# Optimization experiments

Measured on AMD Instinct MI355X. Metric: run time of the kernel, lower is better.

Reference implementation:

```python
import jax, jax.numpy as jnp
import numpy as np

GRID = 112  # densepose predictor output resolution (hardcoded in forward)
D = 16      # CSE embedding dim (view(16, -1) in forward)


def setup_inputs() -> dict:
    key = jax.random.key(0)
    k1, k2 = jax.random.split(key)
    feats = jax.random.normal(k1, (2, D, GRID, GRID), dtype=jnp.float32)
    vertex_embeddings = jax.random.normal(k2, (27554, D), dtype=jnp.float32)
    return {"feats": feats, "vertex_embeddings": vertex_embeddings}


def reference(feats, vertex_embeddings):
    # feats: [B, 16, 112, 112]; vertex_embeddings: [M, 16]
    B = feats.shape[0]
    # per-pixel embeddings: [B, N, D] with N = 112*112 (matches feats[i].view(16,-1).T)
    x = feats.reshape(B, D, -1).transpose(0, 2, 1)
    x2 = jnp.sum(x * x, axis=-1, keepdims=True)            # [B, N, 1]
    v2 = jnp.sum(vertex_embeddings * vertex_embeddings, -1)  # [M]
    dist = x2 - 2.0 * jnp.einsum('bnd,md->bnm', x, vertex_embeddings) + v2
    dps = jnp.argmin(dist, axis=-1).reshape(B, GRID, GRID)  # [B, 112, 112] int
    return feats, dps
```

## Files before the change

kernel.cpp:

```cpp
#include <hip/hip_runtime.h>
#include <math.h>
#include <float.h>

#define GRIDP 112
#define NPIX (GRIDP * GRIDP)
#define D 16
#define TSA 3200
#define TSB 3072

typedef short s16x8 __attribute__((ext_vector_type(8)));
typedef float f32x16 __attribute__((ext_vector_type(16)));

__device__ inline unsigned short f2bf(float x) {
    unsigned u = __float_as_uint(x);
    u += 0x7fffu + ((u >> 16) & 1u);
    return (unsigned short)(u >> 16);
}
__device__ inline float bf2f(unsigned short b) { return __uint_as_float(((unsigned)b) << 16); }

#define MFMA __builtin_amdgcn_mfma_f32_32x32x16_bf16

__global__ __launch_bounds__(256) void prep_verts(
    const float* __restrict__ verts, char* __restrict__ abuf,
    float* __restrict__ v2p, int M, int Mtiles)
{
    int mp = blockIdx.x * 256 + threadIdx.x;
    if (mp >= Mtiles * 32) return;
    int tile = mp >> 5, row = mp & 31;
    float x[D]; float v2;
    if (mp < M) {
        const float4* r4 = (const float4*)(verts + (size_t)mp * D);
        float4 a = r4[0], b = r4[1], c = r4[2], d = r4[3];
        x[0]=a.x; x[1]=a.y; x[2]=a.z; x[3]=a.w;
        x[4]=b.x; x[5]=b.y; x[6]=b.z; x[7]=b.w;
        x[8]=c.x; x[9]=c.y; x[10]=c.z; x[11]=c.w;
        x[12]=d.x; x[13]=d.y; x[14]=d.z; x[15]=d.w;
        float s = 0.f;
#pragma unroll
        for (int e = 0; e < D; ++e) s = fmaf(x[e], x[e], s);
        v2 = s;
        v2p[mp] = s;
    } else {
#pragma unroll
        for (int e = 0; e < D; ++e) x[e] = 0.f;
        v2 = FLT_MAX;
    }
    size_t tb = (size_t)tile * TSA;
    int hv = (row >> 2) & 1, rv = (row & 3) + 4 * (row >> 3);
    *(float*)(abuf + tb + 3072 + hv * 64 + rv * 4) = v2;
#pragma unroll
    for (int e = 0; e < D; ++e) {
        float v = x[e];
        unsigned short t0 = f2bf(v);  float r1 = v - bf2f(t0);
        unsigned short t1 = f2bf(r1); float r2 = r1 - bf2f(t1);
        unsigned short t2 = f2bf(r2);
        size_t o = tb + (size_t)(e >> 3) * 512 + (size_t)row * 16 + (size_t)(e & 7) * 2;
        *(unsigned short*)(abuf + o)        = t0;
        *(unsigned short*)(abuf + o + 1024) = t1;
        *(unsigned short*)(abuf + o + 2048) = t2;
    }
}

__global__ __launch_bounds__(256) void prep_pixels(
    const float* __restrict__ feats, char* __restrict__ bbuf, int NP, int PTiles)
{
    int p = blockIdx.x * 256 + threadIdx.x;
    if (p >= PTiles * 32) return;
    int tile = p >> 5, colr = p & 31;
    float x[D];
    if (p < NP) {
        int b = p / NPIX, n = p - b * NPIX;
        const float* xf = feats + ((size_t)b * D) * NPIX + n;
#pragma unroll
        for (int e = 0; e < D; ++e) x[e] = -2.0f * xf[(size_t)e * NPIX];
    } else {
#pragma unroll
        for (int e = 0; e < D; ++e) x[e] = 0.f;
    }
    size_t tb = (size_t)tile * TSB;
#pragma unroll
    for (int e = 0; e < D; ++e) {
        float v = x[e];
        unsigned short t0 = f2bf(v);  float r1 = v - bf2f(t0);
        unsigned short t1 = f2bf(r1); float r2 = r1 - bf2f(t1);
        unsigned short t2 = f2bf(r2);
        size_t o = tb + (size_t)(e >> 3) * 512 + (size_t)colr * 16 + (size_t)(e & 7) * 2;
        *(unsigned short*)(bbuf + o)        = t0;
        *(unsigned short*)(bbuf + o + 1024) = t1;
        *(unsigned short*)(bbuf + o + 2048) = t2;
    }
}

__device__ inline float mintree16(const f32x16& a) {
    float a0 = fminf(fminf(a[0],  a[1]),  a[2]);
    float a1 = fminf(fminf(a[3],  a[4]),  a[5]);
    float a2 = fminf(fminf(a[6],  a[7]),  a[8]);
    float a3 = fminf(fminf(a[9],  a[10]), a[11]);
    float a4 = fminf(fminf(a[12], a[13]), a[14]);
    float a5 = fminf(fminf(a0, a1), a[15]);
    float a6 = fminf(fminf(a2, a3), a4);
    return fminf(a5, a6);
}

__global__ __launch_bounds__(256) void mfma_scan(
    const char* __restrict__ abuf, const char* __restrict__ bbuf,
    float* __restrict__ pval, int* __restrict__ ptile,
    int Mtiles, int chunk, int NP, int PTiles)
{
    int lane = threadIdx.x & 63;
    int wid  = threadIdx.x >> 6;
    int col  = lane & 31, h = lane >> 5;
    int pt0  = (blockIdx.x * 4 + wid) * 2;
    if (pt0 >= PTiles) return;
    int  pt1  = pt0 + 1;
    bool has1 = pt1 < PTiles;
    int  pt1c = has1 ? pt1 : pt0;

    const char* bb0 = bbuf + (size_t)pt0  * TSB + (size_t)h * 512 + (size_t)col * 16;
    const char* bb1 = bbuf + (size_t)pt1c * TSB + (size_t)h * 512 + (size_t)col * 16;
    s16x8 b0h = *(const s16x8*)bb0;
    s16x8 b0m = *(const s16x8*)(bb0 + 1024);
    s16x8 b0l = *(const s16x8*)(bb0 + 2048);
    s16x8 b1h = *(const s16x8*)bb1;
    s16x8 b1m = *(const s16x8*)(bb1 + 1024);
    s16x8 b1l = *(const s16x8*)(bb1 + 2048);

    int mt0 = blockIdx.y * chunk;
    int mt1 = mt0 + chunk; if (mt1 > Mtiles) mt1 = Mtiles;

    float best0 = FLT_MAX, best1 = FLT_MAX;
    int   t0 = mt0, t1 = mt0;

    const char* ap = abuf + (size_t)mt0 * TSA + (size_t)h * 512 + (size_t)col * 16;
    const char* vp = abuf + (size_t)mt0 * TSA + 3072 + (size_t)h * 64;

#pragma unroll 2
    for (int mt = mt0; mt < mt1; ++mt) {
        s16x8 ah = *(const s16x8*)ap;
        s16x8 am = *(const s16x8*)(ap + 1024);
        s16x8 al = *(const s16x8*)(ap + 2048);
        f32x16 c = *(const f32x16*)vp;
        f32x16 acc0 = c, acc1 = c;
        acc0 = MFMA(ah, b0h, acc0, 0, 0, 0);  acc1 = MFMA(ah, b1h, acc1, 0, 0, 0);
        acc0 = MFMA(ah, b0m, acc0, 0, 0, 0);  acc1 = MFMA(ah, b1m, acc1, 0, 0, 0);
        acc0 = MFMA(am, b0h, acc0, 0, 0, 0);  acc1 = MFMA(am, b1h, acc1, 0, 0, 0);
        acc0 = MFMA(ah, b0l, acc0, 0, 0, 0);  acc1 = MFMA(ah, b1l, acc1, 0, 0, 0);
        acc0 = MFMA(am, b0m, acc0, 0, 0, 0);  acc1 = MFMA(am, b1m, acc1, 0, 0, 0);
        acc0 = MFMA(al, b0h, acc0, 0, 0, 0);  acc1 = MFMA(al, b1h, acc1, 0, 0, 0);
        float m0 = mintree16(acc0);
        float m1 = mintree16(acc1);
        if (m0 < best0) { t0 = mt; best0 = m0; }
        if (m1 < best1) { t1 = mt; best1 = m1; }
        ap += TSA; vp += TSA;
    }

    float o0 = __shfl_xor(best0, 32, 64); int ot0 = __shfl_xor(t0, 32, 64);
    if (o0 < best0 || (o0 == best0 && ot0 < t0)) { best0 = o0; t0 = ot0; }
    float o1 = __shfl_xor(best1, 32, 64); int ot1 = __shfl_xor(t1, 32, 64);
    if (o1 < best1 || (o1 == best1 && ot1 < t1)) { best1 = o1; t1 = ot1; }

    if (lane < 32) {
        int s = blockIdx.y;
        int px0 = pt0 * 32 + col;
        if (px0 < NP) { pval[(size_t)s * NP + px0] = best0; ptile[(size_t)s * NP + px0] = t0; }
        if (has1) {
            int px1 = pt1 * 32 + col;
            if (px1 < NP) { pval[(size_t)s * NP + px1] = best1; ptile[(size_t)s * NP + px1] = t1; }
        }
    }
}

__global__ __launch_bounds__(256) void finalize(
    const float* __restrict__ pval, const int* __restrict__ ptile,
    const float* __restrict__ feats, const float* __restrict__ verts,
    const float* __restrict__ v2p, float* __restrict__ dps,
    int S, int NP, int M)
{
    int p = blockIdx.x * 256 + threadIdx.x;
    if (p >= NP) return;
    float bv = pval[p]; int bt = ptile[p];
    for (int s = 1; s < S; ++s) {
        float v = pval[(size_t)s * NP + p];
        int   t = ptile[(size_t)s * NP + p];
        if (v < bv || (v == bv && t < bt)) { bv = v; bt = t; }
    }
    int b = p / NPIX, n = p - b * NPIX;
    const float* xf = feats + ((size_t)b * D) * NPIX + n;
    float xs[D];
#pragma unroll
    for (int d2 = 0; d2 < D; ++d2) xs[d2] = -2.0f * xf[(size_t)d2 * NPIX];
    int m0 = bt * 32, m1 = m0 + 32; if (m1 > M) m1 = M;
    float best = FLT_MAX; int bi = m0;
    for (int m = m0; m < m1; ++m) {
        const float4* vr = (const float4*)(verts + (size_t)m * D);
        float4 a = vr[0], bq = vr[1], c = vr[2], d = vr[3];
        float acc = v2p[m];
        acc = fmaf(a.x, xs[0], acc);  acc = fmaf(a.y, xs[1], acc);
        acc = fmaf(a.z, xs[2], acc);  acc = fmaf(a.w, xs[3], acc);
        acc = fmaf(bq.x, xs[4], acc); acc = fmaf(bq.y, xs[5], acc);
        acc = fmaf(bq.z, xs[6], acc); acc = fmaf(bq.w, xs[7], acc);
        acc = fmaf(c.x, xs[8], acc);  acc = fmaf(c.y, xs[9], acc);
        acc = fmaf(c.z, xs[10], acc); acc = fmaf(c.w, xs[11], acc);
        acc = fmaf(d.x, xs[12], acc); acc = fmaf(d.y, xs[13], acc);
        acc = fmaf(d.z, xs[14], acc); acc = fmaf(d.w, xs[15], acc);
        if (acc < best) { best = acc; bi = m; }
    }
    dps[p] = (float)bi;
}

__global__ __launch_bounds__(256) void v2_kernel(const float* __restrict__ verts,
                                                 float* __restrict__ v2, int M) {
    int m = blockIdx.x * 256 + threadIdx.x;
    if (m >= M) return;
    const float4* r = (const float4*)(verts + (size_t)m * D);
    float4 a = r[0], b = r[1], c = r[2], d = r[3];
    v2[m] = ((a.x*a.x + a.y*a.y) + (a.z*a.z + a.w*a.w))
          + ((b.x*b.x + b.y*b.y) + (b.z*b.z + b.w*b.w))
          + ((c.x*c.x + c.y*c.y) + (c.z*c.z + c.w*c.w))
          + ((d.x*d.x + d.y*d.y) + (d.z*d.z + d.w*d.w));
}

__global__ __launch_bounds__(256) void argmin_partial(
    const float* __restrict__ feats, const float* __restrict__ verts,
    const float* __restrict__ v2, float* __restrict__ pval, int* __restrict__ pidx,
    int M, int NPtot, int chunk)
{
    int p = blockIdx.x * 256 + threadIdx.x;
    if (p >= NPtot) return;
    int b = p / NPIX, n = p - b * NPIX;
    const float* xf = feats + ((size_t)b * D) * NPIX + n;
    float x[D];
#pragma unroll
    for (int d2 = 0; d2 < D; ++d2) x[d2] = -2.0f * xf[(size_t)d2 * NPIX];
    int s = blockIdx.y;
    int m0 = s * chunk, m1 = m0 + chunk; if (m1 > M) m1 = M;
    float best = INFINITY; int bi = 0;
    for (int m = m0; m < m1; ++m) {
        const float* vr = verts + (size_t)m * D;
        float acc = v2[m];
#pragma unroll
        for (int d2 = 0; d2 < D; ++d2) acc = fmaf(vr[d2], x[d2], acc);
        if (acc < best) { best = acc; bi = m; }
    }
    pval[(size_t)s * NPtot + p] = best;
    pidx[(size_t)s * NPtot + p] = bi;
}

__global__ __launch_bounds__(256) void reduce_idx(
    const float* __restrict__ pval, const int* __restrict__ pidx,
    float* __restrict__ dps, int S, int NP)
{
    int p = blockIdx.x * 256 + threadIdx.x;
    if (p >= NP) return;
    float bv = pval[p]; int bi = pidx[p];
    for (int s = 1; s < S; ++s) {
        float v = pval[(size_t)s * NP + p];
        int   i = pidx[(size_t)s * NP + p];
        if (v < bv || (v == bv && i < bi)) { bv = v; bi = i; }
    }
    dps[p] = (float)bi;
}

extern "C" void kernel_launch(void* const* d_in, const int* in_sizes, int n_in,
                              void* d_out, int out_size, void* d_ws, size_t ws_size,
                              hipStream_t stream)
{
    const float* feats = (const float*)d_in[0];
    const float* verts = (const float*)d_in[1];
    int M          = in_sizes[1] / D;
    int feat_elems = in_sizes[0];
    int Bn         = feat_elems / (D * NPIX);
    int NP         = Bn * NPIX;
    float* out = (float*)d_out;

    hipMemcpyAsync(out, feats, (size_t)feat_elems * sizeof(float),
                   hipMemcpyDeviceToDevice, stream);

    int PTiles = (NP + 31) >> 5;
    int Mtiles = (M + 31) >> 5;

    size_t off = 0;
    auto alloc = [&](size_t sz) { size_t o = off; off = (off + sz + 255) & ~(size_t)255; return o; };
    size_t oBF = alloc((size_t)PTiles * TSB);
    size_t oAF = alloc((size_t)Mtiles * TSA);
    size_t oV2 = alloc((size_t)M * 4);
    size_t base = off;

    int S = 16;
    while (S > 1 && base + (size_t)S * NP * 8 > ws_size) S >>= 1;

    if (base + (size_t)S * NP * 8 <= ws_size) {
        char*  bbuf = (char*)d_ws + oBF;
        char*  abuf = (char*)d_ws + oAF;
        float* v2p  = (float*)((char*)d_ws + oV2);
        float* pval = (float*)((char*)d_ws + base);
        int*   ptil = (int*)((char*)d_ws + base + (size_t)S * NP * 4);

        prep_verts<<<dim3((Mtiles * 32 + 255) / 256), dim3(256), 0, stream>>>(
            verts, abuf, v2p, M, Mtiles);
        prep_pixels<<<dim3((PTiles * 32 + 255) / 256), dim3(256), 0, stream>>>(
            feats, bbuf, NP, PTiles);

        int chunk = (Mtiles + S - 1) / S;
        mfma_scan<<<dim3((PTiles + 7) / 8, S), dim3(256), 0, stream>>>(
            abuf, bbuf, pval, ptil, Mtiles, chunk, NP, PTiles);

        finalize<<<dim3((NP + 255) / 256), dim3(256), 0, stream>>>(
            pval, ptil, feats, verts, v2p, out + feat_elems, S, NP, M);
    } else {
        char* ws = (char*)d_ws;
        float* v2 = (float*)ws;
        size_t o2 = (((size_t)M * 4) + 255) & ~(size_t)255;
        int S2 = 16;
        while (S2 > 1 && o2 + (size_t)S2 * NP * 8 > ws_size) S2 >>= 1;
        float* pval = (float*)(ws + o2);
        int*   pidx = (int*)(ws + o2 + (size_t)S2 * NP * 4);
        int chunk = (M + S2 - 1) / S2;
        v2_kernel<<<dim3((M + 255) / 256), dim3(256), 0, stream>>>(verts, v2, M);
        argmin_partial<<<dim3((NP + 255) / 256, S2), dim3(256), 0, stream>>>(
            feats, verts, v2, pval, pidx, M, NP, chunk);
        reduce_idx<<<dim3((NP + 255) / 256), dim3(256), 0, stream>>>(
            pval, pidx, out + feat_elems, S2, NP);
    }
}
```

Measured before the change: 169.0 us.

## Fuse prep kernels and feats copy into one launch; prefetch next vertex tile

Merges the vertex and pixel preprocessing kernels and the device-to-device copy of feats into a single launch, with block ranges selecting each role. This removes two launches and the separate memcpy. The MFMA scan loop now software-prefetches the next vertex tile's bf16 splits and bias while it computes the current one, hiding global-load latency. To keep the last prefetch in bounds, the A buffer gets one extra padding tile. The prefetch costs extra registers and drops the previous unroll-by-2.

```diff
diff --git a/kernel.cpp b/kernel.cpp
--- a/kernel.cpp
+++ b/kernel.cpp
@@ -10,6 +10,7 @@
 
 typedef short s16x8 __attribute__((ext_vector_type(8)));
 typedef float f32x16 __attribute__((ext_vector_type(16)));
+typedef float f32x4  __attribute__((ext_vector_type(4)));
 
 __device__ inline unsigned short f2bf(float x) {
     unsigned u = __float_as_uint(x);
@@ -20,74 +21,79 @@
 
 #define MFMA __builtin_amdgcn_mfma_f32_32x32x16_bf16
 
-__global__ __launch_bounds__(256) void prep_verts(
-    const float* __restrict__ verts, char* __restrict__ abuf,
-    float* __restrict__ v2p, int M, int Mtiles)
-{
-    int mp = blockIdx.x * 256 + threadIdx.x;
-    if (mp >= Mtiles * 32) return;
-    int tile = mp >> 5, row = mp & 31;
-    float x[D]; float v2;
-    if (mp < M) {
-        const float4* r4 = (const float4*)(verts + (size_t)mp * D);
-        float4 a = r4[0], b = r4[1], c = r4[2], d = r4[3];
-        x[0]=a.x; x[1]=a.y; x[2]=a.z; x[3]=a.w;
-        x[4]=b.x; x[5]=b.y; x[6]=b.z; x[7]=b.w;
-        x[8]=c.x; x[9]=c.y; x[10]=c.z; x[11]=c.w;
-        x[12]=d.x; x[13]=d.y; x[14]=d.z; x[15]=d.w;
-        float s = 0.f;
-#pragma unroll
-        for (int e = 0; e < D; ++e) s = fmaf(x[e], x[e], s);
-        v2 = s;
-        v2p[mp] = s;
+__global__ __launch_bounds__(256) void prep_fused(
+    const float* __restrict__ verts, const float* __restrict__ feats,
+    char* __restrict__ abuf, char* __restrict__ bbuf,
+    float* __restrict__ v2p, float* __restrict__ outf,
+    int M, int Mtiles, int NP, int PTiles, int nvb, int npb, int nf4)
+{
+    int bx = blockIdx.x;
+    if (bx < nvb) {
+        int mp = bx * 256 + threadIdx.x;
+        if (mp >= Mtiles * 32) return;
+        int tile = mp >> 5, row = mp & 31;
+        float x[D]; float v2;
+        if (mp < M) {
+            const float4* r4 = (const float4*)(verts + (size_t)mp * D);
+            float4 a = r4[0], b = r4[1], c = r4[2], d = r4[3];
+            x[0]=a.x; x[1]=a.y; x[2]=a.z; x[3]=a.w;
+            x[4]=b.x; x[5]=b.y; x[6]=b.z; x[7]=b.w;
+            x[8]=c.x; x[9]=c.y; x[10]=c.z; x[11]=c.w;
+            x[12]=d.x; x[13]=d.y; x[14]=d.z; x[15]=d.w;
+            float s = 0.f;
+#pragma unroll
+            for (int e = 0; e < D; ++e) s = fmaf(x[e], x[e], s);
+            v2 = s;
+            v2p[mp] = s;
+        } else {
+#pragma unroll
+            for (int e = 0; e < D; ++e) x[e] = 0.f;
+            v2 = FLT_MAX;
+        }
+        size_t tb = (size_t)tile * TSA;
+        int hv = (row >> 2) & 1, rv = (row & 3) + 4 * (row >> 3);
+        *(float*)(abuf + tb + 3072 + hv * 64 + rv * 4) = v2;
+#pragma unroll
+        for (int e = 0; e < D; ++e) {
+            float v = x[e];
+            unsigned short t0 = f2bf(v);  float r1 = v - bf2f(t0);
+            unsigned short t1 = f2bf(r1); float r2 = r1 - bf2f(t1);
+            unsigned short t2 = f2bf(r2);
+            size_t o = tb + (size_t)(e >> 3) * 512 + (size_t)row * 16 + (size_t)(e & 7) * 2;
+            *(unsigned short*)(abuf + o)        = t0;
+            *(unsigned short*)(abuf + o + 1024) = t1;
+            *(unsigned short*)(abuf + o + 2048) = t2;
+        }
+    } else if (bx < nvb + npb) {
+        int p = (bx - nvb) * 256 + threadIdx.x;
+        if (p >= PTiles * 32) return;
+        int tile = p >> 5, colr = p & 31;
+        float x[D];
+        if (p < NP) {
+            int b = p / NPIX, n = p - b * NPIX;
+            const float* xf = feats + ((size_t)b * D) * NPIX + n;
+#pragma unroll
+            for (int e = 0; e < D; ++e) x[e] = -2.0f * xf[(size_t)e * NPIX];
+        } else {
+#pragma unroll
+            for (int e = 0; e < D; ++e) x[e] = 0.f;
+        }
+        size_t tb = (size_t)tile * TSB;
+#pragma unroll
+        for (int e = 0; e < D; ++e) {
+            float v = x[e];
+            unsigned short t0 = f2bf(v);  float r1 = v - bf2f(t0);
+            unsigned short t1 = f2bf(r1); float r2 = r1 - bf2f(t1);
+            unsigned short t2 = f2bf(r2);
+            size_t o = tb + (size_t)(e >> 3) * 512 + (size_t)colr * 16 + (size_t)(e & 7) * 2;
+            *(unsigned short*)(bbuf + o)        = t0;
+            *(unsigned short*)(bbuf + o + 1024) = t1;
+            *(unsigned short*)(bbuf + o + 2048) = t2;
+        }
     } else {
-#pragma unroll
-        for (int e = 0; e < D; ++e) x[e] = 0.f;
-        v2 = FLT_MAX;
-    }
-    size_t tb = (size_t)tile * TSA;
-    int hv = (row >> 2) & 1, rv = (row & 3) + 4 * (row >> 3);
-    *(float*)(abuf + tb + 3072 + hv * 64 + rv * 4) = v2;
-#pragma unroll
-    for (int e = 0; e < D; ++e) {
-        float v = x[e];
-        unsigned short t0 = f2bf(v);  float r1 = v - bf2f(t0);
-        unsigned short t1 = f2bf(r1); float r2 = r1 - bf2f(t1);
-        unsigned short t2 = f2bf(r2);
-        size_t o = tb + (size_t)(e >> 3) * 512 + (size_t)row * 16 + (size_t)(e & 7) * 2;
-        *(unsigned short*)(abuf + o)        = t0;
-        *(unsigned short*)(abuf + o + 1024) = t1;
-        *(unsigned short*)(abuf + o + 2048) = t2;
-    }
-}
-
-__global__ __launch_bounds__(256) void prep_pixels(
-    const float* __restrict__ feats, char* __restrict__ bbuf, int NP, int PTiles)
-{
-    int p = blockIdx.x * 256 + threadIdx.x;
-    if (p >= PTiles * 32) return;
-    int tile = p >> 5, colr = p & 31;
-    float x[D];
-    if (p < NP) {
-        int b = p / NPIX, n = p - b * NPIX;
-        const float* xf = feats + ((size_t)b * D) * NPIX + n;
-#pragma unroll
-        for (int e = 0; e < D; ++e) x[e] = -2.0f * xf[(size_t)e * NPIX];
-    } else {
-#pragma unroll
-        for (int e = 0; e < D; ++e) x[e] = 0.f;
-    }
-    size_t tb = (size_t)tile * TSB;
-#pragma unroll
-    for (int e = 0; e < D; ++e) {
-        float v = x[e];
-        unsigned short t0 = f2bf(v);  float r1 = v - bf2f(t0);
-        unsigned short t1 = f2bf(r1); float r2 = r1 - bf2f(t1);
-        unsigned short t2 = f2bf(r2);
-        size_t o = tb + (size_t)(e >> 3) * 512 + (size_t)colr * 16 + (size_t)(e & 7) * 2;
-        *(unsigned short*)(bbuf + o)        = t0;
-        *(unsigned short*)(bbuf + o + 1024) = t1;
-        *(unsigned short*)(bbuf + o + 2048) = t2;
+        int i = (bx - nvb - npb) * 256 + threadIdx.x;
+        if (i < nf4)
+            ((float4*)outf)[i] = ((const float4*)feats)[i];
     }
 }
 
@@ -134,12 +140,18 @@
     const char* ap = abuf + (size_t)mt0 * TSA + (size_t)h * 512 + (size_t)col * 16;
     const char* vp = abuf + (size_t)mt0 * TSA + 3072 + (size_t)h * 64;
 
-#pragma unroll 2
+    s16x8 ah = *(const s16x8*)ap;
+    s16x8 am = *(const s16x8*)(ap + 1024);
+    s16x8 al = *(const s16x8*)(ap + 2048);
+    f32x16 c = *(const f32x16*)vp;
+
     for (int mt = mt0; mt < mt1; ++mt) {
-        s16x8 ah = *(const s16x8*)ap;
-        s16x8 am = *(const s16x8*)(ap + 1024);
-        s16x8 al = *(const s16x8*)(ap + 2048);
-        f32x16 c = *(const f32x16*)vp;
+        const char* apn = ap + TSA;
+        s16x8 nah = *(const s16x8*)apn;
+        s16x8 nam = *(const s16x8*)(apn + 1024);
+        s16x8 nal = *(const s16x8*)(apn + 2048);
+        f32x16 nc = *(const f32x16*)(vp + TSA);
+
         f32x16 acc0 = c, acc1 = c;
         acc0 = MFMA(ah, b0h, acc0, 0, 0, 0);  acc1 = MFMA(ah, b1h, acc1, 0, 0, 0);
         acc0 = MFMA(ah, b0m, acc0, 0, 0, 0);  acc1 = MFMA(ah, b1m, acc1, 0, 0, 0);
@@ -151,6 +163,8 @@
         float m1 = mintree16(acc1);
         if (m0 < best0) { t0 = mt; best0 = m0; }
         if (m1 < best1) { t1 = mt; best1 = m1; }
+
+        ah = nah; am = nam; al = nal; c = nc;
         ap += TSA; vp += TSA;
     }
 
@@ -273,16 +287,13 @@
     int NP         = Bn * NPIX;
     float* out = (float*)d_out;
 
-    hipMemcpyAsync(out, feats, (size_t)feat_elems * sizeof(float),
-                   hipMemcpyDeviceToDevice, stream);
-
     int PTiles = (NP + 31) >> 5;
     int Mtiles = (M + 31) >> 5;
 
     size_t off = 0;
     auto alloc = [&](size_t sz) { size_t o = off; off = (off + sz + 255) & ~(size_t)255; return o; };
     size_t oBF = alloc((size_t)PTiles * TSB);
-    size_t oAF = alloc((size_t)Mtiles * TSA);
+    size_t oAF = alloc((size_t)(Mtiles + 1) * TSA);
     size_t oV2 = alloc((size_t)M * 4);
     size_t base = off;
 
@@ -296,10 +307,12 @@
         float* pval = (float*)((char*)d_ws + base);
         int*   ptil = (int*)((char*)d_ws + base + (size_t)S * NP * 4);
 
-        prep_verts<<<dim3((Mtiles * 32 + 255) / 256), dim3(256), 0, stream>>>(
-            verts, abuf, v2p, M, Mtiles);
-        prep_pixels<<<dim3((PTiles * 32 + 255) / 256), dim3(256), 0, stream>>>(
-            feats, bbuf, NP, PTiles);
+        int nvb = (Mtiles * 32 + 255) / 256;
+        int npb = (PTiles * 32 + 255) / 256;
+        int nf4 = feat_elems / 4;
+        int ncb = (nf4 + 255) / 256;
+        prep_fused<<<dim3(nvb + npb + ncb), dim3(256), 0, stream>>>(
+            verts, feats, abuf, bbuf, v2p, out, M, Mtiles, NP, PTiles, nvb, npb, nf4);
 
         int chunk = (Mtiles + S - 1) / S;
         mfma_scan<<<dim3((PTiles + 7) / 8, S), dim3(256), 0, stream>>>(
@@ -308,6 +321,8 @@
         finalize<<<dim3((NP + 255) / 256), dim3(256), 0, stream>>>(
             pval, ptil, feats, verts, v2p, out + feat_elems, S, NP, M);
     } else {
+        hipMemcpyAsync(out, feats, (size_t)feat_elems * sizeof(float),
+                       hipMemcpyDeviceToDevice, stream);
         char* ws = (char*)d_ws;
         float* v2 = (float*)ws;
         size_t o2 = (((size_t)M * 4) + 255) & ~(size_t)255;
```

Result: no change. 170.5 us (+0.9%).
